# Kernel tuning notes

Measured on AMD Instinct MI355X. Metric: run time of the kernel, lower is better.

## Reference

```python
import jax, jax.numpy as jnp
import numpy as np

L = 3          # num_modification_layers
MOD_SCALE = 0.01


def setup_inputs() -> dict:
    key = jax.random.key(0)
    B, E = 8192, 1024
    ks = jax.random.split(key, 12)
    sg = 1.0 / np.sqrt(E)        # GRUCell / Linear(E,.) init bound
    sh = 1.0 / np.sqrt(E // 2)   # Linear(E//2, E) init bound
    u = lambda k, shape, s: jax.random.uniform(k, shape, jnp.float32, -s, s)
    return {
        "x":    jax.random.normal(ks[0], (B, E), jnp.float32),
        # GRUCell params (PyTorch layout: gates ordered r, z, n)
        "W_ih": u(ks[1], (L, 3 * E, E), sg),
        "W_hh": u(ks[2], (L, 3 * E, E), sg),
        "b_ih": u(ks[3], (L, 3 * E), sg),
        "b_hh": u(ks[4], (L, 3 * E), sg),
        # modification network: Linear(E, E//2) -> ReLU -> Linear(E//2, E) -> Tanh
        "W1":   u(ks[5], (L, E // 2, E), sg),
        "b1":   u(ks[6], (L, E // 2), sg),
        "W2":   u(ks[7], (L, E, E // 2), sh),
        "b2":   u(ks[8], (L, E), sh),
        # modification gate: Linear(E, 1) -> Sigmoid
        "Wg":   u(ks[9], (L, 1, E), sg),
        "bg":   u(ks[10], (L, 1), sg),
    }


def reference(x, W_ih, W_hh, b_ih, b_hh, W1, b1, W2, b2, Wg, bg):
    B, E = x.shape
    h_prev = jnp.zeros((B, E), x.dtype)  # hidden states reset to zeros
    cur = x
    for l in range(L):
        # modification network (small MLP) + scalar gate
        sig = jnp.tanh(jax.nn.relu(cur @ W1[l].T + b1[l]) @ W2[l].T + b2[l])  # (B, E)
        gate = jax.nn.sigmoid(cur @ Wg[l].T + bg[l])                           # (B, 1)
        cond = jnp.mean(gate) > 0.5
        # data-dependent self-modification: weight_ih += scale * mean(sig)[None,:]
        # (row-broadcast over the 3E gate rows), predicated on-device
        wih = jnp.where(cond,
                        W_ih[l] + MOD_SCALE * jnp.mean(sig, axis=0)[None, :],
                        W_ih[l])
        # GRUCell (PyTorch semantics)
        gi = cur @ wih.T + b_ih[l]            # (B, 3E)
        gh = h_prev @ W_hh[l].T + b_hh[l]     # (B, 3E) -- h_prev is zeros
        i_r, i_z, i_n = jnp.split(gi, 3, axis=1)
        h_r, h_z, h_n = jnp.split(gh, 3, axis=1)
        r = jax.nn.sigmoid(i_r + h_r)
        z = jax.nn.sigmoid(i_z + h_z)
        n = jnp.tanh(i_n + r * h_n)
        h = (1.0 - z) * n + z * h_prev
        cur = h + sig
    return cur
```

## Files before the change

### kernel.cpp

```cpp
#include <hip/hip_runtime.h>
#include <cstdint>
#include <cstddef>


#define BSZ 8192
#define ESZ 1024

typedef _Float16 f16x8 __attribute__((ext_vector_type(8)));
typedef float    f32x4 __attribute__((ext_vector_type(4)));
typedef unsigned short u16;
typedef u16 u16x4 __attribute__((ext_vector_type(4)));

__device__ __forceinline__ u16 f2h(float f) {
    _Float16 h = (_Float16)f;
    return __builtin_bit_cast(u16, h);
}
__device__ __forceinline__ float h2f(u16 h) {
    return (float)__builtin_bit_cast(_Float16, h);
}

__device__ __forceinline__ void gload16(const void* g, void* l) {
    __builtin_amdgcn_global_load_lds((const __attribute__((address_space(1))) void*)g,
                                     (__attribute__((address_space(3))) void*)l,
                                     16, 0, 0);
}

__device__ __forceinline__ int swzi(int row, int chunk) {
    return (row << 6) + (((chunk ^ row) & 7) << 3);
}

__device__ __forceinline__ float sigmoidf_(float x) {
    return 1.f / (1.f + __expf(-x));
}
__device__ __forceinline__ float tanhf_(float x) {
    float cx = fminf(fmaxf(x, -15.f), 15.f);
    float e = __expf(2.f * cx);
    return (e - 1.f) / (e + 1.f);
}

#define N4_WIH (3 * 3072 * 1024 / 4)
#define N4_W1  (3 * 512 * 1024 / 4)
#define N4_W2  (3 * 1024 * 512 / 4)
#define N4_X   (BSZ * ESZ / 4)

__global__ void cvt_all_kernel(const float* __restrict__ Wih, const float* __restrict__ W1,
                               const float* __restrict__ W2, const float* __restrict__ x,
                               u16* __restrict__ oWih, u16* __restrict__ oW1,
                               u16* __restrict__ oW2, u16* __restrict__ ox) {
    int i = blockIdx.x * 256 + threadIdx.x;
    const float* in;
    u16* out;
    if (i < N4_WIH) { in = Wih; out = oWih; }
    else if (i < N4_WIH + N4_W1) { i -= N4_WIH; in = W1; out = oW1; }
    else if (i < N4_WIH + N4_W1 + N4_W2) { i -= N4_WIH + N4_W1; in = W2; out = oW2; }
    else { i -= N4_WIH + N4_W1 + N4_W2; if (i >= N4_X) return; in = x; out = ox; }
    f32x4 v = ((const f32x4*)in)[i];
    u16x4 o;
    o.x = f2h(v.x); o.y = f2h(v.y); o.z = f2h(v.z); o.w = f2h(v.w);
    ((u16x4*)out)[i] = o;
}

__global__ void gate_kernel(const u16* __restrict__ cur, const float* __restrict__ Wg,
                            const float* __restrict__ bg, const float* __restrict__ colsum,
                            float* __restrict__ gsum, float* __restrict__ sdot) {
    const int wid = threadIdx.x >> 6, lane = threadIdx.x & 63;
    const int row = blockIdx.x * 4 + wid;
    const u16* cr = cur + (size_t)row * ESZ;
    float pg = 0.f, pm = 0.f;
#pragma unroll
    for (int h = 0; h < 2; h++) {
        int base = lane * 16 + h * 8;
        f16x8 cv = *(const f16x8*)(cr + base);
#pragma unroll
        for (int q = 0; q < 2; q++) {
            f32x4 wv = *(const f32x4*)(Wg + base + q * 4);
            f32x4 mv = *(const f32x4*)(colsum + base + q * 4);
#pragma unroll
            for (int e = 0; e < 4; e++) {
                float c = (float)cv[q * 4 + e];
                pg += c * wv[e];
                pm += c * mv[e];
            }
        }
    }
#pragma unroll
    for (int s = 32; s >= 1; s >>= 1) {
        pg += __shfl_xor(pg, s);
        pm += __shfl_xor(pm, s);
    }
    __shared__ float gp[4];
    if (lane == 0) {
        gp[wid] = sigmoidf_(pg + bg[0]);
        sdot[row] = pm * (0.01f / 8192.f);
    }
    __syncthreads();
    if (threadIdx.x == 0) atomicAdd(gsum, gp[0] + gp[1] + gp[2] + gp[3]);
}

template <int NG, int EPI>
__global__ void __launch_bounds__(512, 2) gemm_fused_kernel(
    const u16* __restrict__ A, const u16* __restrict__ W,
    const float* __restrict__ bias, const float* __restrict__ bhh,
    const u16* __restrict__ sig, const float* __restrict__ sdot,
    const float* __restrict__ gsum, u16* __restrict__ outp,
    float* __restrict__ curf_out, float* __restrict__ colsum,
    int K, int NC) {
    __shared__ u16 lA[2][256 * 64];
    __shared__ u16 lB[2][NG][64 * 64];
    const int t = threadIdx.x;
    const int xcd = blockIdx.x & 7, q = blockIdx.x >> 3;
    const int m0 = (xcd * 4 + (q & 3)) * 256;
    const int c0 = (q >> 2) * 64;
    const int wid = t >> 6, lane = t & 63;
    const int waver = wid >> 1, wavec = wid & 1;
    const int lrow = lane & 15, lk = lane >> 4;
    const int E = ESZ;

    f32x4 acc[4][2 * NG] = {};

    auto STAGE = [&](int buf, int k0) {
#pragma unroll
        for (int i = 0; i < 4; i++) {
            int eo = i * 4096 + t * 8;
            int r = eo >> 6;
            int gc = (((eo >> 3) ^ r) & 7) << 3;
            gload16(A + (size_t)(m0 + r) * K + k0 + gc, &lA[buf][eo]);
        }
#pragma unroll
        for (int g = 0; g < NG; g++) {
            int eo = t * 8;
            int r = eo >> 6;
            int gc = (((eo >> 3) ^ r) & 7) << 3;
            gload16(W + (size_t)(g * 1024 + c0 + r) * K + k0 + gc, &lB[buf][g][eo]);
        }
    };

    STAGE(0, 0);
    const int nk = K >> 6;
    int cur = 0;
    for (int kt = 0; kt < nk; ++kt) {
        __syncthreads();
        if (kt + 1 < nk) STAGE(cur ^ 1, (kt + 1) * 64);
#pragma unroll
        for (int kk = 0; kk < 2; kk++) {
            f16x8 af[4];
#pragma unroll
            for (int m = 0; m < 4; m++)
                af[m] = *(const f16x8*)&lA[cur][swzi(waver * 64 + m * 16 + lrow, kk * 4 + lk)];
#pragma unroll
            for (int g = 0; g < NG; g++) {
#pragma unroll
                for (int n = 0; n < 2; n++) {
                    f16x8 bf = *(const f16x8*)&lB[cur][g][swzi(wavec * 32 + n * 16 + lrow, kk * 4 + lk)];
#pragma unroll
                    for (int m = 0; m < 4; m++)
                        acc[m][g * 2 + n] =
                            __builtin_amdgcn_mfma_f32_16x16x32_f16(af[m], bf, acc[m][g * 2 + n], 0, 0, 0);
                }
            }
        }
        cur ^= 1;
    }

    if (EPI == 2) {
        const bool cond = (*gsum) > 4096.f;
#pragma unroll
        for (int m = 0; m < 4; m++) {
            int rbase = m0 + waver * 64 + m * 16 + lk * 4;
            float corr[4];
#pragma unroll
            for (int j = 0; j < 4; j++) corr[j] = cond ? sdot[rbase + j] : 0.f;
#pragma unroll
            for (int n = 0; n < 2; n++) {
                int c = c0 + wavec * 32 + n * 16 + lrow;
                float br = bias[c], bz = bias[E + c], bn = bias[2 * E + c];
                float hr = bhh[c], hz = bhh[E + c], hn = bhh[2 * E + c];
#pragma unroll
                for (int j = 0; j < 4; j++) {
                    float ir = acc[m][0 + n][j] + br + corr[j];
                    float iz = acc[m][2 + n][j] + bz + corr[j];
                    float inn = acc[m][4 + n][j] + bn + corr[j];
                    float r = sigmoidf_(ir + hr);
                    float z = sigmoidf_(iz + hz);
                    float nn = tanhf_(inn + r * hn);
                    float h = (1.f - z) * nn;
                    float o = h + h2f(sig[(size_t)(rbase + j) * E + c]);
                    if (curf_out) curf_out[(size_t)(rbase + j) * E + c] = o;
                    if (outp) outp[(size_t)(rbase + j) * E + c] = f2h(o);
                }
            }
        }
    } else {
        const int N = NC << 6;
#pragma unroll
        for (int n = 0; n < 2; n++) {
            int c = c0 + wavec * 32 + n * 16 + lrow;
            float bv = bias[c];
            float cs = 0.f;
#pragma unroll
            for (int m = 0; m < 4; m++) {
                int rbase = m0 + waver * 64 + m * 16 + lk * 4;
#pragma unroll
                for (int j = 0; j < 4; j++) {
                    float v = acc[m][n][j] + bv;
                    if (EPI == 0) {
                        v = v > 0.f ? v : 0.f;
                        outp[(size_t)(rbase + j) * N + c] = f2h(v);
                    } else {
                        float tv = tanhf_(v);
                        outp[(size_t)(rbase + j) * N + c] = f2h(tv);
                        cs += tv;
                    }
                }
            }
            if (EPI == 1) {
                cs += __shfl_xor(cs, 16);
                cs += __shfl_xor(cs, 32);
                if (lane < 16) atomicAdd(&colsum[c], cs);
            }
        }
    }
}

extern "C" void kernel_launch(void* const* d_in, const int* in_sizes, int n_in,
                              void* d_out, int out_size, void* d_ws, size_t ws_size,
                              hipStream_t stream) {
    const float* x   = (const float*)d_in[0];
    const float* Wih = (const float*)d_in[1];
    const float* bih = (const float*)d_in[3];
    const float* bhh = (const float*)d_in[4];
    const float* W1  = (const float*)d_in[5];
    const float* b1  = (const float*)d_in[6];
    const float* W2  = (const float*)d_in[7];
    const float* b2  = (const float*)d_in[8];
    const float* Wg  = (const float*)d_in[9];
    const float* bg  = (const float*)d_in[10];
    float* out = (float*)d_out;

    char* w = (char*)d_ws;
    u16* Wihb  = (u16*)w;  w += (size_t)3 * 3072 * 1024 * 2;
    u16* W1b   = (u16*)w;  w += (size_t)3 * 512 * 1024 * 2;
    u16* W2b   = (u16*)w;  w += (size_t)3 * 1024 * 512 * 2;
    u16* curbA = (u16*)w;  w += (size_t)BSZ * ESZ * 2;
    u16* curbB = (u16*)w;  w += (size_t)BSZ * ESZ * 2;
    u16* Amat  = (u16*)w;  w += (size_t)BSZ * 512 * 2;
    u16* sigb  = (u16*)w;  w += (size_t)BSZ * ESZ * 2;
    float* colsum = (float*)w;  w += 4096;
    float* gsum   = (float*)w;  w += 256;
    float* sdot   = (float*)w;  w += (size_t)BSZ * 4;

    {
        int n4 = N4_WIH + N4_W1 + N4_W2 + N4_X;
        cvt_all_kernel<<<dim3((n4 + 255) / 256), 256, 0, stream>>>(
            Wih, W1, W2, x, Wihb, W1b, W2b, curbA);
    }

    u16* cin = curbA;
    u16* cout = curbB;
    for (int l = 0; l < 3; l++) {
        hipMemsetAsync(colsum, 0, 4096 + 4, stream);
        gemm_fused_kernel<1, 0><<<dim3(32 * 8), 512, 0, stream>>>(
            cin, W1b + (size_t)l * 512 * 1024, b1 + l * 512, nullptr,
            nullptr, nullptr, nullptr, Amat, nullptr, nullptr, 1024, 8);
        gemm_fused_kernel<1, 1><<<dim3(32 * 16), 512, 0, stream>>>(
            Amat, W2b + (size_t)l * 1024 * 512, b2 + l * 1024, nullptr,
            nullptr, nullptr, nullptr, sigb, nullptr, colsum, 512, 16);
        gate_kernel<<<dim3(BSZ / 4), 256, 0, stream>>>(
            cin, Wg + l * 1024, bg + l, colsum, gsum, sdot);
        gemm_fused_kernel<3, 2><<<dim3(32 * 16), 512, 0, stream>>>(
            cin, Wihb + (size_t)l * 3072 * 1024, bih + l * 3072, bhh + l * 3072,
            sigb, sdot, gsum, (l < 2) ? cout : nullptr,
            (l == 2) ? out : nullptr, nullptr, 1024, 16);
        u16* tmp = cin; cin = cout; cout = tmp;
    }
}
```

Baseline: 581.0 us.

## Rewrite GEMM as 4-stage async LDS pipeline with per-GEMM templated tiles

```diff
diff --git a/kernel.cpp b/kernel.cpp
--- a/kernel.cpp
+++ b/kernel.cpp
@@ -25,8 +25,15 @@
                                      16, 0, 0);
 }
 
-__device__ __forceinline__ int swzi(int row, int chunk) {
-    return (row << 6) + (((chunk ^ row) & 7) << 3);
+template <int N>
+__device__ __forceinline__ void vwait() {
+    if constexpr (N == 0)       asm volatile("s_waitcnt vmcnt(0)" ::: "memory");
+    else if constexpr (N == 3)  asm volatile("s_waitcnt vmcnt(3)" ::: "memory");
+    else if constexpr (N == 4)  asm volatile("s_waitcnt vmcnt(4)" ::: "memory");
+    else if constexpr (N == 5)  asm volatile("s_waitcnt vmcnt(5)" ::: "memory");
+    else if constexpr (N == 6)  asm volatile("s_waitcnt vmcnt(6)" ::: "memory");
+    else if constexpr (N == 8)  asm volatile("s_waitcnt vmcnt(8)" ::: "memory");
+    else if constexpr (N == 10) asm volatile("s_waitcnt vmcnt(10)" ::: "memory");
 }
 
 __device__ __forceinline__ float sigmoidf_(float x) {
@@ -97,84 +104,91 @@
     if (threadIdx.x == 0) atomicAdd(gsum, gp[0] + gp[1] + gp[2] + gp[3]);
 }
 
-template <int NG, int EPI>
-__global__ void __launch_bounds__(512, 2) gemm_fused_kernel(
+template <int BMF, int NG, int NK, int LPS, int PPX, int CW, int K, int EPI>
+__global__ void __launch_bounds__(256, 2) gemm_p4_kernel(
     const u16* __restrict__ A, const u16* __restrict__ W,
     const float* __restrict__ bias, const float* __restrict__ bhh,
     const u16* __restrict__ sig, const float* __restrict__ sdot,
     const float* __restrict__ gsum, u16* __restrict__ outp,
-    float* __restrict__ curf_out, float* __restrict__ colsum,
-    int K, int NC) {
-    __shared__ u16 lA[2][256 * 64];
-    __shared__ u16 lB[2][NG][64 * 64];
+    float* __restrict__ curf_out, float* __restrict__ colsum, int N) {
+    constexpr int BM = BMF * 32;
+    __shared__ u16 lA[4][BM * 32];
+    __shared__ u16 lB[4][NG * 64 * 32];
     const int t = threadIdx.x;
     const int xcd = blockIdx.x & 7, q = blockIdx.x >> 3;
-    const int m0 = (xcd * 4 + (q & 3)) * 256;
-    const int c0 = (q >> 2) * 64;
+    const int m0 = (xcd * PPX + (q % PPX)) * BM;
+    const int c0 = (q / PPX) * CW;
     const int wid = t >> 6, lane = t & 63;
     const int waver = wid >> 1, wavec = wid & 1;
     const int lrow = lane & 15, lk = lane >> 4;
-    const int E = ESZ;
-
-    f32x4 acc[4][2 * NG] = {};
+
+    f32x4 acc[BMF][2 * NG] = {};
 
     auto STAGE = [&](int buf, int k0) {
 #pragma unroll
-        for (int i = 0; i < 4; i++) {
-            int eo = i * 4096 + t * 8;
-            int r = eo >> 6;
-            int gc = (((eo >> 3) ^ r) & 7) << 3;
-            gload16(A + (size_t)(m0 + r) * K + k0 + gc, &lA[buf][eo]);
+        for (int i = 0; i < BMF / 2; i++) {
+            int ci = i * 256 + t;
+            int r = ci >> 2;
+            int slot = (ci ^ r ^ (r >> 2)) & 3;
+            gload16(A + (size_t)(m0 + r) * K + k0 + slot * 8, &lA[buf][ci * 8]);
+        }
+#pragma unroll
+        for (int i = 0; i < NG; i++) {
+            int ci = i * 256 + t;
+            int r = ci >> 2;
+            int g = r >> 6, rl = r & 63;
+            int wrow = (EPI == 2) ? (g * 1024 + c0 + rl) : (c0 + g * 64 + rl);
+            int slot = (ci ^ r ^ (r >> 2)) & 3;
+            gload16(W + (size_t)wrow * K + k0 + slot * 8, &lB[buf][ci * 8]);
+        }
+    };
+
+    STAGE(0, 0);
+    STAGE(1, 32);
+    STAGE(2, 64);
+    for (int kt = 0; kt < NK; ++kt) {
+        if (kt <= NK - 3) vwait<2 * LPS>();
+        else if (kt == NK - 2) vwait<LPS>();
+        else vwait<0>();
+        asm volatile("s_waitcnt lgkmcnt(0)" ::: "memory");
+        __builtin_amdgcn_sched_barrier(0);
+        __builtin_amdgcn_s_barrier();
+        __builtin_amdgcn_sched_barrier(0);
+        if (kt + 4 <= NK) STAGE((kt + 3) & 3, (kt + 3) * 32);
+        const int cb = kt & 3;
+        f16x8 af[BMF];
+#pragma unroll
+        for (int m = 0; m < BMF; m++) {
+            int ar = waver * (BMF * 16) + m * 16 + lrow;
+            af[m] = *(const f16x8*)&lA[cb][ar * 32 + ((lk ^ ar ^ (ar >> 2)) & 3) * 8];
         }
 #pragma unroll
         for (int g = 0; g < NG; g++) {
-            int eo = t * 8;
-            int r = eo >> 6;
-            int gc = (((eo >> 3) ^ r) & 7) << 3;
-            gload16(W + (size_t)(g * 1024 + c0 + r) * K + k0 + gc, &lB[buf][g][eo]);
-        }
-    };
-
-    STAGE(0, 0);
-    const int nk = K >> 6;
-    int cur = 0;
-    for (int kt = 0; kt < nk; ++kt) {
-        __syncthreads();
-        if (kt + 1 < nk) STAGE(cur ^ 1, (kt + 1) * 64);
-#pragma unroll
-        for (int kk = 0; kk < 2; kk++) {
-            f16x8 af[4];
-#pragma unroll
-            for (int m = 0; m < 4; m++)
-                af[m] = *(const f16x8*)&lA[cur][swzi(waver * 64 + m * 16 + lrow, kk * 4 + lk)];
-#pragma unroll
-            for (int g = 0; g < NG; g++) {
-#pragma unroll
-                for (int n = 0; n < 2; n++) {
-                    f16x8 bf = *(const f16x8*)&lB[cur][g][swzi(wavec * 32 + n * 16 + lrow, kk * 4 + lk)];
-#pragma unroll
-                    for (int m = 0; m < 4; m++)
-                        acc[m][g * 2 + n] =
-                            __builtin_amdgcn_mfma_f32_16x16x32_f16(af[m], bf, acc[m][g * 2 + n], 0, 0, 0);
-                }
-            }
-        }
-        cur ^= 1;
-    }
-
-    if (EPI == 2) {
+#pragma unroll
+            for (int n = 0; n < 2; n++) {
+                int br = g * 64 + wavec * 32 + n * 16 + lrow;
+                f16x8 bf = *(const f16x8*)&lB[cb][br * 32 + ((lk ^ br ^ (br >> 2)) & 3) * 8];
+#pragma unroll
+                for (int m = 0; m < BMF; m++)
+                    acc[m][g * 2 + n] =
+                        __builtin_amdgcn_mfma_f32_16x16x32_f16(af[m], bf, acc[m][g * 2 + n], 0, 0, 0);
+            }
+        }
+    }
+
+    if constexpr (EPI == 2) {
         const bool cond = (*gsum) > 4096.f;
 #pragma unroll
-        for (int m = 0; m < 4; m++) {
-            int rbase = m0 + waver * 64 + m * 16 + lk * 4;
+        for (int m = 0; m < BMF; m++) {
+            int rbase = m0 + waver * (BMF * 16) + m * 16 + lk * 4;
             float corr[4];
 #pragma unroll
             for (int j = 0; j < 4; j++) corr[j] = cond ? sdot[rbase + j] : 0.f;
 #pragma unroll
             for (int n = 0; n < 2; n++) {
                 int c = c0 + wavec * 32 + n * 16 + lrow;
-                float br = bias[c], bz = bias[E + c], bn = bias[2 * E + c];
-                float hr = bhh[c], hz = bhh[E + c], hn = bhh[2 * E + c];
+                float br = bias[c], bz = bias[1024 + c], bn = bias[2048 + c];
+                float hr = bhh[c], hz = bhh[1024 + c], hn = bhh[2048 + c];
 #pragma unroll
                 for (int j = 0; j < 4; j++) {
                     float ir = acc[m][0 + n][j] + br + corr[j];
@@ -183,40 +197,41 @@
                     float r = sigmoidf_(ir + hr);
                     float z = sigmoidf_(iz + hz);
                     float nn = tanhf_(inn + r * hn);
-                    float h = (1.f - z) * nn;
-                    float o = h + h2f(sig[(size_t)(rbase + j) * E + c]);
-                    if (curf_out) curf_out[(size_t)(rbase + j) * E + c] = o;
-                    if (outp) outp[(size_t)(rbase + j) * E + c] = f2h(o);
+                    float o = (1.f - z) * nn + h2f(sig[(size_t)(rbase + j) * 1024 + c]);
+                    if (curf_out) curf_out[(size_t)(rbase + j) * 1024 + c] = o;
+                    if (outp) outp[(size_t)(rbase + j) * 1024 + c] = f2h(o);
                 }
             }
         }
     } else {
-        const int N = NC << 6;
-#pragma unroll
-        for (int n = 0; n < 2; n++) {
-            int c = c0 + wavec * 32 + n * 16 + lrow;
-            float bv = bias[c];
-            float cs = 0.f;
-#pragma unroll
-            for (int m = 0; m < 4; m++) {
-                int rbase = m0 + waver * 64 + m * 16 + lk * 4;
-#pragma unroll
-                for (int j = 0; j < 4; j++) {
-                    float v = acc[m][n][j] + bv;
-                    if (EPI == 0) {
-                        v = v > 0.f ? v : 0.f;
-                        outp[(size_t)(rbase + j) * N + c] = f2h(v);
-                    } else {
-                        float tv = tanhf_(v);
-                        outp[(size_t)(rbase + j) * N + c] = f2h(tv);
-                        cs += tv;
+#pragma unroll
+        for (int g = 0; g < NG; g++) {
+#pragma unroll
+            for (int n = 0; n < 2; n++) {
+                int c = c0 + g * 64 + wavec * 32 + n * 16 + lrow;
+                float bv = bias[c];
+                float cs = 0.f;
+#pragma unroll
+                for (int m = 0; m < BMF; m++) {
+                    int rbase = m0 + waver * (BMF * 16) + m * 16 + lk * 4;
+#pragma unroll
+                    for (int j = 0; j < 4; j++) {
+                        float v = acc[m][g * 2 + n][j] + bv;
+                        if (EPI == 0) {
+                            v = v > 0.f ? v : 0.f;
+                            outp[(size_t)(rbase + j) * N + c] = f2h(v);
+                        } else {
+                            float tv = tanhf_(v);
+                            outp[(size_t)(rbase + j) * N + c] = f2h(tv);
+                            cs += tv;
+                        }
                     }
                 }
-            }
-            if (EPI == 1) {
-                cs += __shfl_xor(cs, 16);
-                cs += __shfl_xor(cs, 32);
-                if (lane < 16) atomicAdd(&colsum[c], cs);
+                if (EPI == 1) {
+                    cs += __shfl_xor(cs, 16);
+                    cs += __shfl_xor(cs, 32);
+                    if (lane < 16) atomicAdd(&colsum[c], cs);
+                }
             }
         }
     }
@@ -259,18 +274,18 @@
     u16* cout = curbB;
     for (int l = 0; l < 3; l++) {
         hipMemsetAsync(colsum, 0, 4096 + 4, stream);
-        gemm_fused_kernel<1, 0><<<dim3(32 * 8), 512, 0, stream>>>(
+        gemm_p4_kernel<2, 2, 32, 3, 16, 128, 1024, 0><<<dim3(512), 256, 0, stream>>>(
             cin, W1b + (size_t)l * 512 * 1024, b1 + l * 512, nullptr,
-            nullptr, nullptr, nullptr, Amat, nullptr, nullptr, 1024, 8);
-        gemm_fused_kernel<1, 1><<<dim3(32 * 16), 512, 0, stream>>>(
+            nullptr, nullptr, nullptr, Amat, nullptr, nullptr, 512);
+        gemm_p4_kernel<4, 2, 16, 4, 8, 128, 512, 1><<<dim3(512), 256, 0, stream>>>(
             Amat, W2b + (size_t)l * 1024 * 512, b2 + l * 1024, nullptr,
-            nullptr, nullptr, nullptr, sigb, nullptr, colsum, 512, 16);
+            nullptr, nullptr, nullptr, sigb, nullptr, colsum, 1024);
         gate_kernel<<<dim3(BSZ / 4), 256, 0, stream>>>(
             cin, Wg + l * 1024, bg + l, colsum, gsum, sdot);
-        gemm_fused_kernel<3, 2><<<dim3(32 * 16), 512, 0, stream>>>(
+        gemm_p4_kernel<4, 3, 32, 5, 8, 64, 1024, 2><<<dim3(1024), 256, 0, stream>>>(
             cin, Wihb + (size_t)l * 3072 * 1024, bih + l * 3072, bhh + l * 3072,
             sigb, sdot, gsum, (l < 2) ? cout : nullptr,
-            (l == 2) ? out : nullptr, nullptr, 1024, 16);
+            (l == 2) ? out : nullptr, nullptr, 1024);
         u16* tmp = cin; cin = cout; cout = tmp;
     }
 }
```

Result: slower. 607.2 us (+4.5%).
